# Kernel optimization log

Hardware: AMD Instinct MI355X
Metric: run time of the kernel (lower is better)

The kernel has to match this reference:

```python
import jax, jax.numpy as jnp
import numpy as np

B, T, D, H, L, E, K = 4, 1024, 1024, 16, 2, 8, 2
HD = D // H                      # head_dim = 64
HALF = HD // 2                   # rope half dim = 32
CAP = int(np.ceil(2.0 * B * T / E))  # capacity factor 2 -> 1024
EPS = 1e-5


def build_sin_cos(seq_len, half_dim):
    pos = jnp.arange(seq_len, dtype=jnp.float32)[:, None]
    inv_freq = 1.0 / (10000.0 ** (jnp.arange(0, half_dim * 2, 2, dtype=jnp.float32) / (half_dim * 2)))
    ang = pos * inv_freq                      # (T, half_dim)
    return jnp.sin(ang), jnp.cos(ang)


def layernorm(x, g, b):
    mu = jnp.mean(x, -1, keepdims=True)
    var = jnp.mean(jnp.square(x - mu), -1, keepdims=True)
    return (x - mu) * jax.lax.rsqrt(var + EPS) * g + b


def attention(x, qkv_w, proj_w, sin, cos):
    # x: (B,T,D)
    qkv = (x @ qkv_w).reshape(B, T, H, 3 * HD)
    q, k, v = jnp.split(qkv, 3, axis=-1)      # each (B,T,H,HD)
    s = sin[None, :, None, :]                 # (1,T,1,HALF)
    c = cos[None, :, None, :]
    def rope(t):
        t1, t2 = t[..., :HALF], t[..., HALF:]
        return jnp.concatenate([t1 * c - t2 * s, t1 * s + t2 * c], axis=-1)
    q, k = rope(q), rope(k)
    scores = jnp.einsum('bqhd,bkhd->bhqk', q, k) / jnp.sqrt(jnp.float32(HD)).astype(x.dtype)
    causal = jnp.tril(jnp.ones((T, T), dtype=bool))
    scores = jnp.where(causal, scores, jnp.asarray(-1e9, scores.dtype))
    probs = jax.nn.softmax(scores, axis=-1)
    out = jnp.einsum('bhqk,bkhd->bqhd', probs, v).reshape(B, T, D)
    return out @ proj_w


def sparse_moe(x, gate_w, w1, b1, w2, b2):
    # eval mode: no router noise, aux_loss = 0
    flat = x.reshape(-1, D)                   # (N, D)
    N = flat.shape[0]
    gates = jax.nn.softmax((flat @ gate_w).astype(jnp.float32), axis=-1)  # (N, E)
    _, inds = jax.lax.top_k(gates, K)         # (N, K)
    mask = jnp.zeros((N, E), dtype=bool).at[jnp.arange(N)[:, None], inds].set(True)
    pos = jnp.cumsum(mask.astype(jnp.int32), axis=0) * mask - 1
    keep = (pos < CAP) & mask                 # (N, E) capacity-truncated assignment
    keepT = keep.T                            # (E, N)
    # stable argsort puts kept tokens first, preserving token order
    order = jnp.argsort(~keepT, axis=1)[:, :CAP]           # (E, CAP)
    valid = jnp.take_along_axis(keepT, order, axis=1)      # (E, CAP)
    safe = jnp.where(valid, order, 0)
    xg = flat[safe]                                        # (E, CAP, D)
    gv = jnp.take_along_axis(gates.T, safe, axis=1) * valid  # (E, CAP)
    h = jax.nn.gelu(jnp.einsum('ecd,edh->ech', xg, w1) + b1[:, None, :], approximate=False)
    out = jnp.einsum('ech,ehd->ecd', h, w2) + b2[:, None, :]
    contrib = out * gv[..., None].astype(flat.dtype)
    scatter_idx = jnp.where(valid, order, N)               # out-of-range -> dropped
    final = jnp.zeros_like(flat).at[scatter_idx.reshape(-1)].add(
        contrib.reshape(-1, D), mode='drop')
    return final.reshape(x.shape)


def setup_inputs() -> dict:
    key = jax.random.key(0)
    ks = jax.random.split(key, 8)
    s = 0.02
    return {
        'x': jax.random.normal(ks[0], (B, T, D), jnp.float32),
        'ln1_g': jnp.ones((L, D), jnp.float32),
        'ln1_b': jnp.zeros((L, D), jnp.float32),
        'qkv_w': jax.random.normal(ks[1], (L, D, 3 * D), jnp.float32) * s,
        'proj_w': jax.random.normal(ks[2], (L, D, D), jnp.float32) * s,
        'ln2_g': jnp.ones((L, D), jnp.float32),
        'ln2_b': jnp.zeros((L, D), jnp.float32),
        'gate_w': jax.random.normal(ks[3], (L, D, E), jnp.float32) * s,
        'w1': jax.random.normal(ks[4], (L, E, D, 4 * D), jnp.float32) * s,
        'b1': jnp.zeros((L, E, 4 * D), jnp.float32),
        'w2': jax.random.normal(ks[5], (L, E, 4 * D, D), jnp.float32) * s,
        'b2': jnp.zeros((L, E, D), jnp.float32),
    }


def reference(x, ln1_g, ln1_b, qkv_w, proj_w, ln2_g, ln2_b, gate_w, w1, b1, w2, b2):
    sin, cos = build_sin_cos(T, HALF)
    for l in range(L):
        x = x + attention(layernorm(x, ln1_g[l], ln1_b[l]), qkv_w[l], proj_w[l], sin, cos)
        x = x + sparse_moe(layernorm(x, ln2_g[l], ln2_b[l]), gate_w[l], w1[l], b1[l], w2[l], b2[l])
    return x
```

## Files before the change

kernel.cpp:

```cpp
#include <hip/hip_runtime.h>
#include <cstdint>

#define DD 1024
#define TT 1024
#define BB 4
#define HH 16
#define EE 8
#define NTOK 4096
#define CAPS 1024

using f16 = _Float16;
using f16x8 = __attribute__((ext_vector_type(8))) _Float16;
using f16x4 = __attribute__((ext_vector_type(4))) _Float16;
using f32x4 = __attribute__((ext_vector_type(4))) float;

#define MFMA16(a, b, c) __builtin_amdgcn_mfma_f32_16x16x32_f16(a, b, c, 0, 0, 0)

__device__ __forceinline__ void gload16(const void* g, void* l) {
  __builtin_amdgcn_global_load_lds((const __attribute__((address_space(1))) unsigned int*)g,
                                   (__attribute__((address_space(3))) unsigned int*)l, 16, 0, 0);
}

__device__ __forceinline__ void split2(float v, f16& h, f16& lo) {
  h = (f16)v;
  lo = (f16)((v - (float)h) * 2048.0f);
}

__device__ __forceinline__ void split_store(f16* ph, f16* pl, float v) {
  f16 h = (f16)v;
  *ph = h;
  *pl = (f16)((v - (float)h) * 2048.0f);
}

__global__ void splitT_k(const float* __restrict__ src, f16* __restrict__ dh, f16* __restrict__ dl,
                         int R, int C, long sSrc, long sDst) {
  __shared__ float tile[32][33];
  long z = blockIdx.z;
  src += z * sSrc; dh += z * sDst; dl += z * sDst;
  int c0 = blockIdx.x * 32, r0 = blockIdx.y * 32;
  int tx = threadIdx.x, ty = threadIdx.y;
  #pragma unroll
  for (int i = 0; i < 4; ++i) {
    int r = ty + i * 8;
    tile[r][tx] = src[(long)(r0 + r) * C + c0 + tx];
  }
  __syncthreads();
  #pragma unroll
  for (int i = 0; i < 4; ++i) {
    int cc = ty + i * 8;
    float v = tile[tx][cc];
    long idx = (long)(c0 + cc) * R + r0 + tx;
    f16 h, lo; split2(v, h, lo);
    dh[idx] = h; dl[idx] = lo;
  }
}

template<bool GATE>
__launch_bounds__(256)
__global__ void ln_k(const float* __restrict__ x, const float* __restrict__ g, const float* __restrict__ b,
                     f16* __restrict__ oh, f16* __restrict__ ol,
                     const float* __restrict__ gw, float* __restrict__ gates) {
  int row = blockIdx.x, tid = threadIdx.x;
  int lane = tid & 63, wid = tid >> 6;
  __shared__ float red[4];
  __shared__ float pg[4][8];
  __shared__ float logits[8];
  const float* xr = x + (long)row * DD;
  int col = tid * 4;
  float4 v = *(const float4*)(xr + col);
  float s = v.x + v.y + v.z + v.w;
  #pragma unroll
  for (int off = 32; off >= 1; off >>= 1) s += __shfl_down(s, off);
  if (lane == 0) red[wid] = s;
  __syncthreads();
  float mu = (red[0] + red[1] + red[2] + red[3]) * (1.0f / DD);
  float d0 = v.x - mu, d1 = v.y - mu, d2 = v.z - mu, d3 = v.w - mu;
  float sq = d0 * d0 + d1 * d1 + d2 * d2 + d3 * d3;
  __syncthreads();
  #pragma unroll
  for (int off = 32; off >= 1; off >>= 1) sq += __shfl_down(sq, off);
  if (lane == 0) red[wid] = sq;
  __syncthreads();
  float var = (red[0] + red[1] + red[2] + red[3]) * (1.0f / DD);
  float rstd = rsqrtf(var + 1e-5f);
  float xv[4];
  xv[0] = d0 * rstd * g[col] + b[col];
  xv[1] = d1 * rstd * g[col + 1] + b[col + 1];
  xv[2] = d2 * rstd * g[col + 2] + b[col + 2];
  xv[3] = d3 * rstd * g[col + 3] + b[col + 3];
  f16x4 hv, lv;
  #pragma unroll
  for (int j = 0; j < 4; ++j) { f16 h, lo; split2(xv[j], h, lo); hv[j] = h; lv[j] = lo; }
  *(f16x4*)(oh + (long)row * DD + col) = hv;
  *(f16x4*)(ol + (long)row * DD + col) = lv;
  if (GATE) {
    float part[8];
    #pragma unroll
    for (int e = 0; e < 8; ++e) part[e] = 0.0f;
    #pragma unroll
    for (int j = 0; j < 4; ++j) {
      const float* gwr = gw + (long)(col + j) * 8;
      #pragma unroll
      for (int e = 0; e < 8; ++e) part[e] += xv[j] * gwr[e];
    }
    #pragma unroll
    for (int off = 32; off >= 1; off >>= 1) {
      #pragma unroll
      for (int e = 0; e < 8; ++e) part[e] += __shfl_down(part[e], off);
    }
    if (lane == 0) {
      #pragma unroll
      for (int e = 0; e < 8; ++e) pg[wid][e] = part[e];
    }
    __syncthreads();
    if (tid < 8) logits[tid] = pg[0][tid] + pg[1][tid] + pg[2][tid] + pg[3][tid];
    __syncthreads();
    if (tid < 8) {
      float mx = logits[0];
      #pragma unroll
      for (int e2 = 1; e2 < 8; ++e2) mx = fmaxf(mx, logits[e2]);
      float den = 0.0f;
      #pragma unroll
      for (int e2 = 0; e2 < 8; ++e2) den += expf(logits[e2] - mx);
      gates[(long)row * 8 + tid] = expf(logits[tid] - mx) / den;
    }
  }
}

__global__ void sincos_k(float* st, float* ct) {
  int i = blockIdx.x * 256 + threadIdx.x;
  if (i >= TT * 32) return;
  int t = i >> 5, f = i & 31;
  float inv = powf(10000.0f, -(float)f * (1.0f / 32.0f));
  float ang = (float)t * inv;
  st[i] = sinf(ang);
  ct[i] = cosf(ang);
}

__launch_bounds__(256)
__global__ void rope_split_k(const float* __restrict__ qkv, const float* __restrict__ st, const float* __restrict__ ct,
                             f16* __restrict__ qh, f16* __restrict__ ql,
                             f16* __restrict__ kh, f16* __restrict__ kl,
                             f16* __restrict__ vth, f16* __restrict__ vtl) {
  int bx = blockIdx.x;
  int bh = bx >> 4, t0 = (bx & 15) * 64;
  int b = bh >> 4, hh = bh & 15;
  int tid = threadIdx.x;
  {
    int r = tid >> 2, quarter = tid & 3;
    int t = t0 + r;
    const float* rowp = qkv + ((long)(b * TT + t)) * 3072 + hh * 192;
    long obase = ((long)bh * TT + t) * 64;
    #pragma unroll
    for (int j = 0; j < 8; ++j) {
      int i = quarter * 8 + j;
      float sa = st[t * 32 + i], ca = ct[t * 32 + i];
      float a1 = rowp[i], a2 = rowp[i + 32];
      split_store(qh + obase + i, ql + obase + i, a1 * ca - a2 * sa);
      split_store(qh + obase + i + 32, ql + obase + i + 32, a1 * sa + a2 * ca);
      float c1 = rowp[64 + i], c2 = rowp[96 + i];
      split_store(kh + obase + i, kl + obase + i, c1 * ca - c2 * sa);
      split_store(kh + obase + i + 32, kl + obase + i + 32, c1 * sa + c2 * ca);
    }
  }
  __shared__ f16 vh_t[64][72];
  __shared__ f16 vl_t[64][72];
  {
    int d = tid & 63, tq = tid >> 6;
    #pragma unroll
    for (int p = 0; p < 16; ++p) {
      int tl = tq * 16 + p;
      float val = qkv[((long)(b * TT + t0 + tl)) * 3072 + hh * 192 + 128 + d];
      f16 h, lo; split2(val, h, lo);
      vh_t[tl][d] = h; vl_t[tl][d] = lo;
    }
  }
  __syncthreads();
  {
    int d = tid >> 2, c = tid & 3;
    long vbase = ((long)bh * 64 + d) * TT + t0 + c * 16;
    f16x8 ph0, ph1, pl0, pl1;
    #pragma unroll
    for (int j = 0; j < 8; ++j) {
      ph0[j] = vh_t[c * 16 + j][d];
      pl0[j] = vl_t[c * 16 + j][d];
      ph1[j] = vh_t[c * 16 + 8 + j][d];
      pl1[j] = vl_t[c * 16 + 8 + j][d];
    }
    *(f16x8*)(vth + vbase) = ph0;
    *(f16x8*)(vth + vbase + 8) = ph1;
    *(f16x8*)(vtl + vbase) = pl0;
    *(f16x8*)(vtl + vbase + 8) = pl1;
  }
}

__launch_bounds__(256, 2)
__global__ void attn_k(const f16* __restrict__ qh, const f16* __restrict__ ql,
                       const f16* __restrict__ kh, const f16* __restrict__ kl,
                       const f16* __restrict__ vth, const f16* __restrict__ vtl,
                       f16* __restrict__ oh_out, f16* __restrict__ ol_out) {
  __shared__ __align__(16) f16 KsH[4096], KsL[4096], VsH[4096], VsL[4096];
  __shared__ __align__(16) f16 Pw[4][2][2048];
  int bx = blockIdx.x;
  int bh = bx & 63;
  int qt = (int)((0x31204657u >> ((bx >> 6) << 2)) & 7u);
  int tid = threadIdx.x;
  int wid = tid >> 6, lane = tid & 63;
  int lr = lane & 15, lg = lane >> 4;
  long bhT = (long)bh * TT;
  int qrow0 = qt * 128 + wid * 32;
  int qend = qrow0 + 32;

  f16x8 qfh[2][2], qfl[2][2];
  #pragma unroll
  for (int qi = 0; qi < 2; ++qi) {
    long qoff = (bhT + qrow0 + qi * 16 + lr) * 64 + lg * 8;
    qfh[qi][0] = *(const f16x8*)(qh + qoff);
    qfh[qi][1] = *(const f16x8*)(qh + qoff + 32);
    qfl[qi][0] = *(const f16x8*)(ql + qoff);
    qfl[qi][1] = *(const f16x8*)(ql + qoff + 32);
  }

  f32x4 o_hi[2][4], o_md[2][4];
  #pragma unroll
  for (int qi = 0; qi < 2; ++qi)
    #pragma unroll
    for (int dj = 0; dj < 4; ++dj) {
      o_hi[qi][dj] = {0.f, 0.f, 0.f, 0.f};
      o_md[qi][dj] = {0.f, 0.f, 0.f, 0.f};
    }
  float m[2][4], lsum[2][4];
  #pragma unroll
  for (int qi = 0; qi < 2; ++qi)
    #pragma unroll
    for (int r = 0; r < 4; ++r) { m[qi][r] = -1e30f; lsum[qi][r] = 0.0f; }

  int srow = tid >> 3, slot = tid & 7;
  int gc = ((slot ^ (srow & 7)) << 3);
  const f16* kHp = kh + (bhT + srow) * 64 + gc;
  const f16* kLp = kl + (bhT + srow) * 64 + gc;
  const f16* vHp = vth + ((long)bh * 64 + srow) * TT + gc;
  const f16* vLp = vtl + ((long)bh * 64 + srow) * TT + gc;
  int t8 = tid * 8;
  int rsw = lr & 7;
  int c0 = ((lg ^ rsw) << 3), c1 = (((4 | lg) ^ rsw) << 3);
  f16* Ph = Pw[wid][0];
  f16* Pl = Pw[wid][1];

  int ntiles = 2 * (qt + 1);
  for (int kb = 0; kb < ntiles; ++kb) {
    int kv0 = kb * 64;
    gload16(kHp + (long)kv0 * 64, KsH + t8);
    gload16(kHp + (long)(kv0 + 32) * 64, KsH + 2048 + t8);
    gload16(kLp + (long)kv0 * 64, KsL + t8);
    gload16(kLp + (long)(kv0 + 32) * 64, KsL + 2048 + t8);
    gload16(vHp + kv0, VsH + t8);
    gload16(vHp + (long)32 * TT + kv0, VsH + 2048 + t8);
    gload16(vLp + kv0, VsL + t8);
    gload16(vLp + (long)32 * TT + kv0, VsL + 2048 + t8);
    __syncthreads();

    if (kv0 < qend) {
      f32x4 s[2][4];
      #pragma unroll
      for (int kj = 0; kj < 4; ++kj) {
        int rb = (kj * 16 + lr) * 64;
        f16x8 kfh0 = *(const f16x8*)(KsH + rb + c0);
        f16x8 kfh1 = *(const f16x8*)(KsH + rb + c1);
        f16x8 kfl0 = *(const f16x8*)(KsL + rb + c0);
        f16x8 kfl1 = *(const f16x8*)(KsL + rb + c1);
        #pragma unroll
        for (int qi = 0; qi < 2; ++qi) {
          f32x4 a = {0.f, 0.f, 0.f, 0.f};
          a = MFMA16(qfh[qi][0], kfh0, a);
          a = MFMA16(qfh[qi][1], kfh1, a);
          a = a * 2048.0f;
          a = MFMA16(qfh[qi][0], kfl0, a);
          a = MFMA16(qfh[qi][1], kfl1, a);
          a = MFMA16(qfl[qi][0], kfh0, a);
          a = MFMA16(qfl[qi][1], kfh1, a);
          s[qi][kj] = a;
        }
      }
      const float ss = 0.125f / 2048.0f;
      bool needmask = (kv0 + 64 > qrow0);
      float rm[2][4];
      #pragma unroll
      for (int qi = 0; qi < 2; ++qi)
        #pragma unroll
        for (int r = 0; r < 4; ++r) {
          int qrow = qrow0 + qi * 16 + lg * 4 + r;
          float mx = -1e30f;
          #pragma unroll
          for (int kj = 0; kj < 4; ++kj) {
            float v = s[qi][kj][r] * ss;
            if (needmask && (kv0 + kj * 16 + lr > qrow)) v = -1e9f;
            s[qi][kj][r] = v;
            mx = fmaxf(mx, v);
          }
          rm[qi][r] = mx;
        }
      #pragma unroll
      for (int off = 1; off < 16; off <<= 1)
        #pragma unroll
        for (int qi = 0; qi < 2; ++qi)
          #pragma unroll
          for (int r = 0; r < 4; ++r) rm[qi][r] = fmaxf(rm[qi][r], __shfl_xor(rm[qi][r], off));
      float alpha[2][4], rs[2][4];
      #pragma unroll
      for (int qi = 0; qi < 2; ++qi)
        #pragma unroll
        for (int r = 0; r < 4; ++r) {
          float mn = fmaxf(m[qi][r], rm[qi][r]);
          alpha[qi][r] = __expf(m[qi][r] - mn);
          m[qi][r] = mn;
          rs[qi][r] = 0.0f;
        }
      #pragma unroll
      for (int qi = 0; qi < 2; ++qi)
        #pragma unroll
        for (int kj = 0; kj < 4; ++kj)
          #pragma unroll
          for (int r = 0; r < 4; ++r) {
            float p = __expf(s[qi][kj][r] - m[qi][r]);
            rs[qi][r] += p;
            int prow = qi * 16 + lg * 4 + r;
            int pcol = kj * 16 + lr;
            int idx = prow * 64 + (((pcol >> 3) ^ (prow & 7)) << 3) + (pcol & 7);
            f16 hv = (f16)p;
            Ph[idx] = hv;
            Pl[idx] = (f16)((p - (float)hv) * 2048.0f);
          }
      #pragma unroll
      for (int off = 1; off < 16; off <<= 1)
        #pragma unroll
        for (int qi = 0; qi < 2; ++qi)
          #pragma unroll
          for (int r = 0; r < 4; ++r) rs[qi][r] += __shfl_xor(rs[qi][r], off);
      #pragma unroll
      for (int qi = 0; qi < 2; ++qi)
        #pragma unroll
        for (int r = 0; r < 4; ++r) lsum[qi][r] = lsum[qi][r] * alpha[qi][r] + rs[qi][r];
      #pragma unroll
      for (int qi = 0; qi < 2; ++qi)
        #pragma unroll
        for (int dj = 0; dj < 4; ++dj)
          #pragma unroll
          for (int r = 0; r < 4; ++r) {
            o_hi[qi][dj][r] *= alpha[qi][r];
            o_md[qi][dj][r] *= alpha[qi][r];
          }
      f16x8 pah[2][2], pal[2][2];
      #pragma unroll
      for (int qi = 0; qi < 2; ++qi) {
        int pr = (qi * 16 + lr) * 64;
        pah[qi][0] = *(const f16x8*)(Ph + pr + c0);
        pah[qi][1] = *(const f16x8*)(Ph + pr + c1);
        pal[qi][0] = *(const f16x8*)(Pl + pr + c0);
        pal[qi][1] = *(const f16x8*)(Pl + pr + c1);
      }
      #pragma unroll
      for (int dj = 0; dj < 4; ++dj) {
        int vb = (dj * 16 + lr) * 64;
        f16x8 vh0 = *(const f16x8*)(VsH + vb + c0);
        f16x8 vh1 = *(const f16x8*)(VsH + vb + c1);
        f16x8 vl0 = *(const f16x8*)(VsL + vb + c0);
        f16x8 vl1 = *(const f16x8*)(VsL + vb + c1);
        #pragma unroll
        for (int qi = 0; qi < 2; ++qi) {
          o_hi[qi][dj] = MFMA16(pah[qi][0], vh0, o_hi[qi][dj]);
          o_hi[qi][dj] = MFMA16(pah[qi][1], vh1, o_hi[qi][dj]);
          o_md[qi][dj] = MFMA16(pah[qi][0], vl0, o_md[qi][dj]);
          o_md[qi][dj] = MFMA16(pah[qi][1], vl1, o_md[qi][dj]);
          o_md[qi][dj] = MFMA16(pal[qi][0], vh0, o_md[qi][dj]);
          o_md[qi][dj] = MFMA16(pal[qi][1], vh1, o_md[qi][dj]);
        }
      }
    }
    __syncthreads();
  }

  int b = bh >> 4, hh = bh & 15;
  #pragma unroll
  for (int qi = 0; qi < 2; ++qi)
    #pragma unroll
    for (int r = 0; r < 4; ++r) {
      float invl = 1.0f / lsum[qi][r];
      int qrow = qrow0 + qi * 16 + lg * 4 + r;
      long obase = ((long)(b * TT + qrow)) * DD + hh * 64 + lr;
      #pragma unroll
      for (int dj = 0; dj < 4; ++dj) {
        float val = (o_hi[qi][dj][r] + o_md[qi][dj][r] * (1.0f / 2048.0f)) * invl;
        f16 hv = (f16)val;
        oh_out[obase + dj * 16] = hv;
        ol_out[obase + dj * 16] = (f16)((val - (float)hv) * 2048.0f);
      }
    }
}

template<int EPI, bool SPLIT>
__launch_bounds__(256, 2)
__global__ void gemmF(const f16* __restrict__ Ah, const f16* __restrict__ Al, long sA,
                      const f16* __restrict__ Bh, const f16* __restrict__ Bl, long sB,
                      int M, int N, int K,
                      float* __restrict__ outF, long sOutF,
                      const float* __restrict__ resid,
                      const float* __restrict__ bias, long sBias,
                      f16* __restrict__ outH, f16* __restrict__ outL, long sOutH) {
  __shared__ __align__(16) f16 pool[(SPLIT ? 4 : 2) * 128 * 64];
  f16* AsH = pool;
  f16* BsH = pool + 8192;
  f16* AsL = SPLIT ? pool + 16384 : pool;
  f16* BsL = SPLIT ? pool + 24576 : pool;

  int z = blockIdx.z;
  int bn = blockIdx.x, bm = blockIdx.y;
  int tid = threadIdx.x;
  int wid = tid >> 6, lane = tid & 63;
  int wm = (wid >> 1) * 64, wn = (wid & 1) * 64;
  int lr = lane & 15, lg = lane >> 4;

  f32x4 aH[4][4], aL[4][4];
  #pragma unroll
  for (int i = 0; i < 4; ++i)
    #pragma unroll
    for (int j = 0; j < 4; ++j) {
      aH[i][j] = {0.f, 0.f, 0.f, 0.f};
      if (SPLIT) aL[i][j] = {0.f, 0.f, 0.f, 0.f};
    }

  int srow = tid >> 3;
  int gcol = (((tid & 7) ^ (srow & 7)) << 3);
  const f16* apH = Ah + (long)z * sA + ((long)(bm * 128 + srow)) * K + gcol;
  const f16* bpH = Bh + (long)z * sB + ((long)(bn * 128 + srow)) * K + gcol;
  const f16* apL = nullptr; const f16* bpL = nullptr;
  if (SPLIT) {
    apL = Al + (long)z * sA + ((long)(bm * 128 + srow)) * K + gcol;
    bpL = Bl + (long)z * sB + ((long)(bn * 128 + srow)) * K + gcol;
  }
  int tid8 = tid * 8;
  int rsw = lr & 7;

  for (int kt = 0; kt < K; kt += 64) {
    #pragma unroll
    for (int r4 = 0; r4 < 4; ++r4) {
      long go = (long)kt + (long)(r4 * 32) * K;
      int lo = tid8 + r4 * 2048;
      gload16(apH + go, AsH + lo);
      gload16(bpH + go, BsH + lo);
      if (SPLIT) {
        gload16(apL + go, AsL + lo);
        gload16(bpL + go, BsL + lo);
      }
    }
    __syncthreads();
    #pragma unroll
    for (int kk2 = 0; kk2 < 2; ++kk2) {
      int sws = (((kk2 << 2) | lg) ^ rsw) << 3;
      f16x8 afH[4], afL[4];
      #pragma unroll
      for (int i = 0; i < 4; ++i) {
        int ro = (wm + i * 16 + lr) * 64 + sws;
        afH[i] = *(const f16x8*)(AsH + ro);
        if (SPLIT) afL[i] = *(const f16x8*)(AsL + ro);
      }
      #pragma unroll
      for (int j = 0; j < 4; ++j) {
        int ro = (wn + j * 16 + lr) * 64 + sws;
        f16x8 bH = *(const f16x8*)(BsH + ro);
        #pragma unroll
        for (int i = 0; i < 4; ++i) aH[i][j] = MFMA16(afH[i], bH, aH[i][j]);
        if (SPLIT) {
          f16x8 bL = *(const f16x8*)(BsL + ro);
          #pragma unroll
          for (int i = 0; i < 4; ++i) {
            aL[i][j] = MFMA16(afH[i], bL, aL[i][j]);
            aL[i][j] = MFMA16(afL[i], bH, aL[i][j]);
          }
        }
      }
    }
    __syncthreads();
  }

  #pragma unroll
  for (int i = 0; i < 4; ++i) {
    #pragma unroll
    for (int j = 0; j < 4; ++j) {
      #pragma unroll
      for (int r = 0; r < 4; ++r) {
        int row = bm * 128 + wm + i * 16 + lg * 4 + r;
        int col = bn * 128 + wn + j * 16 + lr;
        float v = aH[i][j][r];
        if (SPLIT) v += aL[i][j][r] * (1.0f / 2048.0f);
        if (EPI == 0) {
          outF[(long)row * N + col] = v;
        } else if (EPI == 1) {
          long idx = (long)row * N + col;
          outF[idx] = v + resid[idx];
        } else if (EPI == 2) {
          float t = v + bias[(long)z * sBias + col];
          float ge = 0.5f * t * (1.0f + erff(t * 0.70710678118f));
          long idx = (long)z * sOutH + (long)row * N + col;
          f16 hv = (f16)ge;
          outH[idx] = hv;
          if (SPLIT) outL[idx] = (f16)((ge - (float)hv) * 2048.0f);
        } else {
          long idx = (long)z * sOutF + (long)row * N + col;
          outF[idx] = v + bias[(long)z * sBias + col];
        }
      }
    }
  }
}

__launch_bounds__(512)
__global__ void route_k(const float* __restrict__ gates, int* __restrict__ etok, int* __restrict__ slotof) {
  __shared__ unsigned char lmask[NTOK];
  __shared__ unsigned char ltop[NTOK];
  int tid = threadIdx.x;
  for (int t = tid; t < NTOK; t += 512) {
    const float* gr = gates + (long)t * 8;
    float gv[8];
    #pragma unroll
    for (int e = 0; e < 8; ++e) gv[e] = gr[e];
    int e1 = 0; float bv = gv[0];
    #pragma unroll
    for (int e = 1; e < 8; ++e) if (gv[e] > bv) { bv = gv[e]; e1 = e; }
    int e2 = -1; float bv2 = -1e30f;
    #pragma unroll
    for (int e = 0; e < 8; ++e) if (e != e1 && gv[e] > bv2) { bv2 = gv[e]; e2 = e; }
    lmask[t] = (unsigned char)((1u << e1) | (1u << e2));
    ltop[t] = (unsigned char)(e1 | (e2 << 4));
    slotof[t * 2] = -1;
    slotof[t * 2 + 1] = -1;
  }
  __syncthreads();
  int e = tid >> 6, lane = tid & 63;
  int cnt = 0;
  for (int c = 0; c < NTOK / 64; ++c) {
    int t = c * 64 + lane;
    int bit = (lmask[t] >> e) & 1;
    unsigned long long bal = __ballot(bit);
    int pre = __popcll(bal & ((1ull << lane) - 1ull));
    int slot = cnt + pre;
    if (bit && slot < CAPS) {
      etok[e * CAPS + slot] = t;
      int tp = ltop[t];
      int k = ((tp & 15) == e) ? 0 : 1;
      slotof[t * 2 + k] = (e << 16) | slot;
    }
    cnt += __popcll(bal);
  }
  int kept = cnt < CAPS ? cnt : CAPS;
  for (int s = kept + lane; s < CAPS; s += 64) etok[e * CAPS + s] = 0;
}

__global__ void gather_k(const int* __restrict__ etok, const f16* __restrict__ xh, const f16* __restrict__ xl,
                         f16* __restrict__ gh, f16* __restrict__ gl) {
  int es = blockIdx.x, tid = threadIdx.x;
  int tok = etok[es];
  const uint4* s1 = (const uint4*)(xh + (long)tok * DD);
  const uint4* s2 = (const uint4*)(xl + (long)tok * DD);
  ((uint4*)(gh + (long)es * DD))[tid] = s1[tid];
  ((uint4*)(gl + (long)es * DD))[tid] = s2[tid];
}

__global__ void scatter_k(const int* __restrict__ slotof, const float* __restrict__ gates,
                          const float* __restrict__ moe, float* __restrict__ x) {
  int t = blockIdx.x, tid = threadIdx.x;
  int s0 = slotof[t * 2], s1 = slotof[t * 2 + 1];
  float4* xr = (float4*)(x + (long)t * DD);
  float4 v = xr[tid];
  if (s0 >= 0) {
    int e = s0 >> 16, sl = s0 & 0xffff;
    float gv = gates[(long)t * 8 + e];
    float4 mo = ((const float4*)(moe + ((long)e * CAPS + sl) * DD))[tid];
    v.x += gv * mo.x; v.y += gv * mo.y; v.z += gv * mo.z; v.w += gv * mo.w;
  }
  if (s1 >= 0) {
    int e = s1 >> 16, sl = s1 & 0xffff;
    float gv = gates[(long)t * 8 + e];
    float4 mo = ((const float4*)(moe + ((long)e * CAPS + sl) * DD))[tid];
    v.x += gv * mo.x; v.y += gv * mo.y; v.z += gv * mo.z; v.w += gv * mo.w;
  }
  xr[tid] = v;
}

extern "C" void kernel_launch(void* const* d_in, const int* in_sizes, int n_in,
                              void* d_out, int out_size, void* d_ws, size_t ws_size,
                              hipStream_t stream) {
  const float* x_in   = (const float*)d_in[0];
  const float* ln1_g  = (const float*)d_in[1];
  const float* ln1_b  = (const float*)d_in[2];
  const float* qkv_w  = (const float*)d_in[3];
  const float* proj_w = (const float*)d_in[4];
  const float* ln2_g  = (const float*)d_in[5];
  const float* ln2_b  = (const float*)d_in[6];
  const float* gate_w = (const float*)d_in[7];
  const float* w1     = (const float*)d_in[8];
  const float* b1     = (const float*)d_in[9];
  const float* w2     = (const float*)d_in[10];
  const float* b2     = (const float*)d_in[11];
  float* x = (float*)d_out;

  char* p = (char*)d_ws;
  auto alloc = [&](size_t bytes) { char* r = p; p += (bytes + 255) & ~(size_t)255; return (void*)r; };

  f16* Wreg   = (f16*)alloc(134217728);
  float* qkvb = (float*)alloc(4096ull * 3072 * 4);
  f16* qhB  = (f16*)alloc(4194304ull * 2);
  f16* qlB  = (f16*)alloc(4194304ull * 2);
  f16* khB  = (f16*)alloc(4194304ull * 2);
  f16* klB  = (f16*)alloc(4194304ull * 2);
  f16* vthB = (f16*)alloc(4194304ull * 2);
  f16* vtlB = (f16*)alloc(4194304ull * 2);
  f16* xnh  = (f16*)alloc(4194304ull * 2);
  f16* xnl  = (f16*)alloc(4194304ull * 2);
  f16* atth = (f16*)alloc(4194304ull * 2);
  f16* attl = (f16*)alloc(4194304ull * 2);
  f16* xgh  = (f16*)alloc(8388608ull * 2);
  f16* xgl  = (f16*)alloc(8388608ull * 2);
  f16* hhB  = (f16*)alloc(33554432ull * 2);
  f16* hlB  = (f16*)alloc(33554432ull * 2);
  float* moe = (float*)alloc(8388608ull * 4);
  float* stab = (float*)alloc(32768ull * 4);
  float* ctab = (float*)alloc(32768ull * 4);
  float* gates = (float*)alloc(32768ull * 4);
  int* etok  = (int*)alloc(8192ull * 4);
  int* slotof = (int*)alloc(8192ull * 4);

  f16* qkvTh = Wreg;
  f16* qkvTl = Wreg + 3145728;
  f16* projTh = Wreg + 2 * 3145728;
  f16* projTl = Wreg + 2 * 3145728 + 1048576;
  f16* w1Th = Wreg;
  f16* w1Tl = Wreg + 33554432;
  f16* w2Th = Wreg;
  f16* w2Tl = Wreg + 33554432;

  hipMemcpyAsync(x, x_in, (size_t)NTOK * DD * 4, hipMemcpyDeviceToDevice, stream);
  sincos_k<<<(TT * 32 + 255) / 256, 256, 0, stream>>>(stab, ctab);

  for (int l = 0; l < 2; ++l) {
    splitT_k<<<dim3(3072 / 32, 1024 / 32, 1), dim3(32, 8), 0, stream>>>(
        qkv_w + (long)l * DD * 3072, qkvTh, qkvTl, 1024, 3072, 0, 0);
    splitT_k<<<dim3(1024 / 32, 1024 / 32, 1), dim3(32, 8), 0, stream>>>(
        proj_w + (long)l * DD * DD, projTh, projTl, 1024, 1024, 0, 0);
    ln_k<false><<<NTOK, 256, 0, stream>>>(x, ln1_g + l * DD, ln1_b + l * DD, xnh, xnl, nullptr, nullptr);
    gemmF<0, true><<<dim3(3072 / 128, 4096 / 128, 1), 256, 0, stream>>>(
        xnh, xnl, 0, qkvTh, qkvTl, 0, 4096, 3072, 1024,
        qkvb, 0, nullptr, nullptr, 0, nullptr, nullptr, 0);
    rope_split_k<<<BB * HH * (TT / 64), 256, 0, stream>>>(qkvb, stab, ctab, qhB, qlB, khB, klB, vthB, vtlB);
    attn_k<<<512, 256, 0, stream>>>(qhB, qlB, khB, klB, vthB, vtlB, atth, attl);
    gemmF<1, true><<<dim3(1024 / 128, 4096 / 128, 1), 256, 0, stream>>>(
        atth, attl, 0, projTh, projTl, 0, 4096, 1024, 1024,
        x, 0, x, nullptr, 0, nullptr, nullptr, 0);

    ln_k<true><<<NTOK, 256, 0, stream>>>(x, ln2_g + l * DD, ln2_b + l * DD, xnh, xnl,
                                         gate_w + (long)l * DD * EE, gates);
    route_k<<<1, 512, 0, stream>>>(gates, etok, slotof);
    gather_k<<<EE * CAPS, 128, 0, stream>>>(etok, xnh, xnl, xgh, xgl);
    splitT_k<<<dim3(4096 / 32, 1024 / 32, EE), dim3(32, 8), 0, stream>>>(
        w1 + (long)l * EE * DD * 4096, w1Th, w1Tl, 1024, 4096, (long)DD * 4096, (long)4096 * DD);
    if (l == 0) {
      gemmF<2, true><<<dim3(4096 / 128, 1024 / 128, EE), 256, 0, stream>>>(
          xgh, xgl, (long)CAPS * DD, w1Th, w1Tl, (long)4096 * DD, 1024, 4096, 1024,
          nullptr, 0, nullptr, b1 + (long)l * EE * 4096, 4096, hhB, hlB, (long)CAPS * 4096);
    } else {
      gemmF<2, false><<<dim3(4096 / 128, 1024 / 128, EE), 256, 0, stream>>>(
          xgh, xgl, (long)CAPS * DD, w1Th, w1Tl, (long)4096 * DD, 1024, 4096, 1024,
          nullptr, 0, nullptr, b1 + (long)l * EE * 4096, 4096, hhB, hlB, (long)CAPS * 4096);
    }
    splitT_k<<<dim3(1024 / 32, 4096 / 32, EE), dim3(32, 8), 0, stream>>>(
        w2 + (long)l * EE * 4096 * DD, w2Th, w2Tl, 4096, 1024, (long)4096 * DD, (long)DD * 4096);
    if (l == 0) {
      gemmF<3, true><<<dim3(1024 / 128, 1024 / 128, EE), 256, 0, stream>>>(
          hhB, hlB, (long)CAPS * 4096, w2Th, w2Tl, (long)DD * 4096, 1024, 1024, 4096,
          moe, (long)CAPS * DD, nullptr, b2 + (long)l * EE * DD, DD, nullptr, nullptr, 0);
    } else {
      gemmF<3, false><<<dim3(1024 / 128, 1024 / 128, EE), 256, 0, stream>>>(
          hhB, hlB, (long)CAPS * 4096, w2Th, w2Tl, (long)DD * 4096, 1024, 1024, 4096,
          moe, (long)CAPS * DD, nullptr, b2 + (long)l * EE * DD, DD, nullptr, nullptr, 0);
    }
    scatter_k<<<NTOK, 256, 0, stream>>>(slotof, gates, moe, x);
  }
  (void)in_sizes; (void)n_in; (void)out_size; (void)ws_size;
}
```

Baseline: 1.458 ms.

## Double-buffer GEMM LDS tiles and halve K-tile for split-precision path

Restructures the gemmF main loop into a two-stage software pipeline. The next K-tile is issued via global_load_lds into an alternate LDS buffer while the current tile feeds the MFMAs, and one barrier per iteration replaces two. To keep LDS at 64KB for the split hi/lo variant, that variant's K-tile drops from 64 to 32 with a new swizzle pattern. The non-split variant keeps BK=64 but doubles its LDS to 64KB, which may limit occupancy, and the halved tile doubles iteration count for split GEMMs.

```diff
diff --git a/kernel.cpp b/kernel.cpp
--- a/kernel.cpp
+++ b/kernel.cpp
@@ -407,11 +407,10 @@
                       const float* __restrict__ resid,
                       const float* __restrict__ bias, long sBias,
                       f16* __restrict__ outH, f16* __restrict__ outL, long sOutH) {
-  __shared__ __align__(16) f16 pool[(SPLIT ? 4 : 2) * 128 * 64];
-  f16* AsH = pool;
-  f16* BsH = pool + 8192;
-  f16* AsL = SPLIT ? pool + 16384 : pool;
-  f16* BsL = SPLIT ? pool + 24576 : pool;
+  constexpr int BK = SPLIT ? 32 : 64;
+  constexpr int PSZ = 128 * BK;
+  constexpr int BUF = (SPLIT ? 4 : 2) * PSZ;
+  __shared__ __align__(16) f16 pool[2 * BUF];
 
   int z = blockIdx.z;
   int bn = blockIdx.x, bm = blockIdx.y;
@@ -429,8 +428,14 @@
       if (SPLIT) aL[i][j] = {0.f, 0.f, 0.f, 0.f};
     }
 
-  int srow = tid >> 3;
-  int gcol = (((tid & 7) ^ (srow & 7)) << 3);
+  int srow, gcol;
+  if (SPLIT) {
+    srow = tid >> 2;
+    gcol = (((tid & 3) ^ ((srow >> 1) & 3)) << 3);
+  } else {
+    srow = tid >> 3;
+    gcol = (((tid & 7) ^ (srow & 7)) << 3);
+  }
   const f16* apH = Ah + (long)z * sA + ((long)(bm * 128 + srow)) * K + gcol;
   const f16* bpH = Bh + (long)z * sB + ((long)(bn * 128 + srow)) * K + gcol;
   const f16* apL = nullptr; const f16* bpL = nullptr;
@@ -438,49 +443,81 @@
     apL = Al + (long)z * sA + ((long)(bm * 128 + srow)) * K + gcol;
     bpL = Bl + (long)z * sB + ((long)(bn * 128 + srow)) * K + gcol;
   }
-  int tid8 = tid * 8;
-  int rsw = lr & 7;
-
-  for (int kt = 0; kt < K; kt += 64) {
-    #pragma unroll
-    for (int r4 = 0; r4 < 4; ++r4) {
-      long go = (long)kt + (long)(r4 * 32) * K;
-      int lo = tid8 + r4 * 2048;
-      gload16(apH + go, AsH + lo);
-      gload16(bpH + go, BsH + lo);
-      if (SPLIT) {
-        gload16(apL + go, AsL + lo);
-        gload16(bpL + go, BsL + lo);
+  int t8 = tid * 8;
+
+  auto stage = [&](int b, int kt) {
+    f16* base = pool + b * BUF;
+    if (SPLIT) {
+      #pragma unroll
+      for (int rr = 0; rr < 2; ++rr) {
+        long go = (long)kt + (long)(rr * 64) * K;
+        int lo = t8 + rr * 2048;
+        gload16(apH + go, base + lo);
+        gload16(bpH + go, base + PSZ + lo);
+        gload16(apL + go, base + 2 * PSZ + lo);
+        gload16(bpL + go, base + 3 * PSZ + lo);
+      }
+    } else {
+      #pragma unroll
+      for (int r4 = 0; r4 < 4; ++r4) {
+        long go = (long)kt + (long)(r4 * 32) * K;
+        int lo = t8 + r4 * 2048;
+        gload16(apH + go, base + lo);
+        gload16(bpH + go, base + PSZ + lo);
+      }
+    }
+  };
+
+  int nk = K / BK;
+  stage(0, 0);
+  __syncthreads();
+  int cur = 0;
+  for (int ks = 0; ks < nk; ++ks) {
+    if (ks + 1 < nk) stage(cur ^ 1, (ks + 1) * BK);
+    const f16* AsH = pool + cur * BUF;
+    const f16* BsH = AsH + PSZ;
+    if (SPLIT) {
+      const f16* AsL = AsH + 2 * PSZ;
+      const f16* BsL = AsH + 3 * PSZ;
+      int sws = ((lg ^ ((lr >> 1) & 3)) << 3);
+      f16x8 afH[4], afL[4];
+      #pragma unroll
+      for (int i = 0; i < 4; ++i) {
+        int ro = (wm + i * 16 + lr) * 32 + sws;
+        afH[i] = *(const f16x8*)(AsH + ro);
+        afL[i] = *(const f16x8*)(AsL + ro);
+      }
+      #pragma unroll
+      for (int j = 0; j < 4; ++j) {
+        int ro = (wn + j * 16 + lr) * 32 + sws;
+        f16x8 bH = *(const f16x8*)(BsH + ro);
+        f16x8 bL = *(const f16x8*)(BsL + ro);
+        #pragma unroll
+        for (int i = 0; i < 4; ++i) {
+          aH[i][j] = MFMA16(afH[i], bH, aH[i][j]);
+          aL[i][j] = MFMA16(afH[i], bL, aL[i][j]);
+          aL[i][j] = MFMA16(afL[i], bH, aL[i][j]);
+        }
+      }
+    } else {
+      int rsw = lr & 7;
+      #pragma unroll
+      for (int kk2 = 0; kk2 < 2; ++kk2) {
+        int sws = (((kk2 << 2) | lg) ^ rsw) << 3;
+        f16x8 afH[4];
+        #pragma unroll
+        for (int i = 0; i < 4; ++i)
+          afH[i] = *(const f16x8*)(AsH + (wm + i * 16 + lr) * 64 + sws);
+        #pragma unroll
+        for (int j = 0; j < 4; ++j) {
+          f16x8 bH = *(const f16x8*)(BsH + (wn + j * 16 + lr) * 64 + sws);
+          #pragma unroll
+          for (int i = 0; i < 4; ++i) aH[i][j] = MFMA16(afH[i], bH, aH[i][j]);
+        }
       }
     }
     __syncthreads();
-    #pragma unroll
-    for (int kk2 = 0; kk2 < 2; ++kk2) {
-      int sws = (((kk2 << 2) | lg) ^ rsw) << 3;
-      f16x8 afH[4], afL[4];
-      #pragma unroll
-      for (int i = 0; i < 4; ++i) {
-        int ro = (wm + i * 16 + lr) * 64 + sws;
-        afH[i] = *(const f16x8*)(AsH + ro);
-        if (SPLIT) afL[i] = *(const f16x8*)(AsL + ro);
-      }
-      #pragma unroll
-      for (int j = 0; j < 4; ++j) {
-        int ro = (wn + j * 16 + lr) * 64 + sws;
-        f16x8 bH = *(const f16x8*)(BsH + ro);
-        #pragma unroll
-        for (int i = 0; i < 4; ++i) aH[i][j] = MFMA16(afH[i], bH, aH[i][j]);
-        if (SPLIT) {
-          f16x8 bL = *(const f16x8*)(BsL + ro);
-          #pragma unroll
-          for (int i = 0; i < 4; ++i) {
-            aL[i][j] = MFMA16(afH[i], bL, aL[i][j]);
-            aL[i][j] = MFMA16(afL[i], bH, aL[i][j]);
-          }
-        }
-      }
-    }
-    __syncthreads();
+    cur ^= 1;
   }
 
   #pragma unroll
```

Result: slower. 1.570 ms (+7.6%).
